# Kernel optimization log

Hardware: AMD Instinct MI355X
Metric: run time of the kernel (lower is better)

## Reference

```python
import jax, jax.numpy as jnp
import numpy as np
import math

HID = 512
HEADS = 8
DK = HID // HEADS
B, S, T = 8, 4096, 512


def setup_inputs() -> dict:
    key = jax.random.key(0)
    ks = jax.random.split(key, 12)
    scale = 0.02
    inp = {
        "inputs": jax.random.normal(ks[0], (B, S, HID), dtype=jnp.float32),
        "targets": jax.random.normal(ks[1], (B, T, HID), dtype=jnp.float32),
        "mask": jnp.ones((B, S), dtype=bool),
        "Wq": jax.random.normal(ks[2], (HID, HID), dtype=jnp.float32) * scale,
        "bq": jnp.zeros((HID,), dtype=jnp.float32),
        "Wk": jax.random.normal(ks[3], (HID, HID), dtype=jnp.float32) * scale,
        "bk": jnp.zeros((HID,), dtype=jnp.float32),
        "Wv": jax.random.normal(ks[4], (HID, HID), dtype=jnp.float32) * scale,
        "bv": jnp.zeros((HID,), dtype=jnp.float32),
        "Wo": jax.random.normal(ks[5], (HID, HID), dtype=jnp.float32) * scale,
        "bo": jnp.zeros((HID,), dtype=jnp.float32),
    }
    return inp


def reference(inputs, targets, mask, Wq, bq, Wk, bk, Wv, bv, Wo, bo):
    # PoolingFunction(method='multihead-attention'), dropout=0 (identity),
    # hidden_size == output_size so mapping_function is identity.
    b, t, h = targets.shape
    s = inputs.shape[1]
    Q = (targets @ Wq.T + bq).reshape(b, t, HEADS, DK)
    K = (inputs @ Wk.T + bk).reshape(b, s, HEADS, DK)
    V = (inputs @ Wv.T + bv).reshape(b, s, HEADS, DK)
    # scores: b x heads x tgt x seq (same math as (Q*K).sum(-1)/sqrt(d_k))
    e = jnp.einsum('bthd,bshd->bhts', Q, K) / math.sqrt(DK)
    neg = (1.0 - mask.astype(jnp.float32)) * -1e20  # b x s
    e = e + neg[:, None, None, :]
    a = jax.nn.softmax(e, axis=-1)  # softmax over seq dim
    ctx = jnp.einsum('bhts,bshd->bthd', a, V).reshape(b, t, h)
    return ctx @ Wo.T + bo
```

## Files before the change

### kernel.cpp

```cpp
#include <hip/hip_runtime.h>
#include <hip/hip_bf16.h>
#include <cstdint>
#include <cstddef>

#define HIDN   512
#define NHEADS 8
#define BATCH  8
#define SLEN   4096
#define TLEN   512
#define SSPLIT 4
#define SCHUNK (SLEN / SSPLIT)
#define SCL2   0.18033688f

typedef __attribute__((ext_vector_type(8))) short   bf16x8;
typedef __attribute__((ext_vector_type(4))) float   f32x4;
typedef unsigned short u16;
typedef unsigned int   u32;

__device__ __forceinline__ u32 pkbf(float a, float b) {
    __hip_bfloat162 h = __float22bfloat162_rn(float2{a, b});
    union { __hip_bfloat162 h; u32 u; } un; un.h = h; return un.u;
}
__device__ __forceinline__ u32 cvtpk(float a, float b) {
    u32 r;
    asm("v_cvt_pk_bf16_f32 %0, %1, %2" : "=v"(r) : "v"(a), "v"(b));
    return r;
}
__device__ __forceinline__ float fexp2(float x) {
    return __builtin_amdgcn_exp2f(x);
}
__device__ __forceinline__ void gload_lds16(const u16* g, u16* l) {
    __builtin_amdgcn_global_load_lds(
        (const __attribute__((address_space(1))) u32*)g,
        (__attribute__((address_space(3))) u32*)l, 16, 0, 0);
}

__global__ __launch_bounds__(256) void cvt_all(
    const float* __restrict__ X, const float* __restrict__ Tg,
    const float* __restrict__ Wq, const float* __restrict__ Wk,
    const float* __restrict__ Wv, const float* __restrict__ Wo,
    const int* __restrict__ mask,
    u16* __restrict__ Xc, u16* __restrict__ Tc, u16* __restrict__ Wc,
    float* __restrict__ negf)
{
    int i4 = blockIdx.x * 256 + threadIdx.x;
    if (i4 >= 4980736) {
        int off = i4 - 4980736;
        int4 mv = ((const int4*)mask)[off];
        float4 nv;
        nv.x = mv.x ? 0.f : -1e30f; nv.y = mv.y ? 0.f : -1e30f;
        nv.z = mv.z ? 0.f : -1e30f; nv.w = mv.w ? 0.f : -1e30f;
        ((float4*)negf)[off] = nv;
        return;
    }
    const float* s; u16* d; long off;
    if (i4 < 4194304)      { s = X;  d = Xc; off = i4; }
    else if (i4 < 4718592) { s = Tg; d = Tc; off = i4 - 4194304; }
    else {
        int wi = i4 - 4718592; int widx = wi >> 16;
        s = (widx == 0) ? Wq : (widx == 1) ? Wk : (widx == 2) ? Wv : Wo;
        d = Wc + widx * 262144; off = wi & 65535;
    }
    float4 v = *(const float4*)(s + off * 4);
    uint2 o; o.x = pkbf(v.x, v.y); o.y = pkbf(v.z, v.w);
    *(uint2*)(d + off * 4) = o;
}


template<int MODE, int SEQ>
__device__ __forceinline__ void gemmA_body(
    const u16* __restrict__ A, const u16* __restrict__ Bw,
    const float* __restrict__ bias, void* __restrict__ Yv,
    int m0, int n0, u16* As, u16* Bs)
{
    const int tid = threadIdx.x;
    const int lane = tid & 63;
    const int w = tid >> 6;
    const int m = lane & 15, qd = lane >> 4;
    const int wm = w >> 1, wn = w & 1;

    f32x4 acc[4][4];
#pragma unroll
    for (int i = 0; i < 4; ++i)
#pragma unroll
        for (int j = 0; j < 4; ++j) acc[i][j] = (f32x4){0.f, 0.f, 0.f, 0.f};

    for (int k0 = 0; k0 < HIDN; k0 += 32) {
#pragma unroll
        for (int r = 0; r < 2; ++r) {
            const int f = tid + r * 256;
            const int row = f >> 2, c8 = (f & 3) * 8;
            const int fb = f & ~63;
            gload_lds16(A  + (size_t)(m0 + row) * HIDN + k0 + c8, As + fb * 8);
            gload_lds16(Bw + (size_t)(n0 + row) * HIDN + k0 + c8, Bs + fb * 8);
        }
        __syncthreads();
        bf16x8 af[4], bf[4];
#pragma unroll
        for (int t = 0; t < 4; ++t) {
            af[t] = *(bf16x8*)&As[(64 * wm + 16 * t + m) * 32 + 8 * qd];
            bf[t] = *(bf16x8*)&Bs[(64 * wn + 16 * t + m) * 32 + 8 * qd];
        }
#pragma unroll
        for (int ti = 0; ti < 4; ++ti)
#pragma unroll
            for (int tj = 0; tj < 4; ++tj)
                acc[ti][tj] = __builtin_amdgcn_mfma_f32_16x16x32_bf16(
                    af[ti], bf[tj], acc[ti][tj], 0, 0, 0);
        __syncthreads();
    }

#pragma unroll
    for (int ti = 0; ti < 4; ++ti) {
        const int gr0 = m0 + 64 * wm + 16 * ti + 4 * qd;
#pragma unroll
        for (int tj = 0; tj < 4; ++tj) {
            const int gcol = n0 + 64 * wn + 16 * tj + m;
            const float bv = bias[gcol];
            if (MODE == 0) {
                float* Y = (float*)Yv;
#pragma unroll
                for (int i = 0; i < 4; ++i)
                    Y[(size_t)(gr0 + i) * HIDN + gcol] = acc[ti][tj][i] + bv;
            } else {
                u16* Y = (u16*)Yv;
                const int b = gr0 / SEQ, h = gcol >> 6, d = gcol & 63;
                const int r = gr0 & (SEQ - 1);
                uint2 o;
                o.x = pkbf(acc[ti][tj][0] + bv, acc[ti][tj][1] + bv);
                o.y = pkbf(acc[ti][tj][2] + bv, acc[ti][tj][3] + bv);
                *(uint2*)&Y[(((size_t)(b * 8 + h)) * 64 + d) * SEQ + r] = o;
            }
        }
    }
}

template<int SEQ>
__device__ __forceinline__ void wxT_body(
    const u16* __restrict__ Wm, const u16* __restrict__ X,
    const float* __restrict__ bias, u16* __restrict__ Y,
    int m0, int n0, u16* As, u16* Bs)
{
    const int tid = threadIdx.x;
    const int lane = tid & 63;
    const int w = tid >> 6;
    const int m = lane & 15, qd = lane >> 4;
    const int wm = w >> 1, wn = w & 1;

    f32x4 acc[4][4];
#pragma unroll
    for (int i = 0; i < 4; ++i)
#pragma unroll
        for (int j = 0; j < 4; ++j) acc[i][j] = (f32x4){0.f, 0.f, 0.f, 0.f};

    for (int k0 = 0; k0 < HIDN; k0 += 32) {
#pragma unroll
        for (int r = 0; r < 2; ++r) {
            const int f = tid + r * 256;
            const int row = f >> 2, c8 = (f & 3) * 8;
            const int fb = f & ~63;
            gload_lds16(Wm + (size_t)(m0 + row) * HIDN + k0 + c8, As + fb * 8);
            gload_lds16(X  + (size_t)(n0 + row) * HIDN + k0 + c8, Bs + fb * 8);
        }
        __syncthreads();
        bf16x8 af[4], bf[4];
#pragma unroll
        for (int t = 0; t < 4; ++t) {
            af[t] = *(bf16x8*)&As[(64 * wm + 16 * t + m) * 32 + 8 * qd];
            bf[t] = *(bf16x8*)&Bs[(64 * wn + 16 * t + m) * 32 + 8 * qd];
        }
#pragma unroll
        for (int ti = 0; ti < 4; ++ti)
#pragma unroll
            for (int tj = 0; tj < 4; ++tj)
                acc[ti][tj] = __builtin_amdgcn_mfma_f32_16x16x32_bf16(
                    af[ti], bf[tj], acc[ti][tj], 0, 0, 0);
        __syncthreads();
    }

#pragma unroll
    for (int ti = 0; ti < 4; ++ti) {
        const int o = m0 + 64 * wm + 16 * ti + 4 * qd;
        const float4 bv = *(const float4*)&bias[o];
        const int h = o >> 6, d0 = o & 63;
#pragma unroll
        for (int tj = 0; tj < 4; ++tj) {
            const int n = n0 + 64 * wn + 16 * tj + m;
            const int b = n / SEQ, r = n & (SEQ - 1);
            uint2 pk;
            pk.x = pkbf(acc[ti][tj][0] + bv.x, acc[ti][tj][1] + bv.y);
            pk.y = pkbf(acc[ti][tj][2] + bv.z, acc[ti][tj][3] + bv.w);
            *(uint2*)&Y[(((size_t)(b * 8 + h)) * SEQ + r) * 64 + d0] = pk;
        }
    }
}

__global__ __launch_bounds__(256)
void proj_all(const u16* __restrict__ Wc, const u16* __restrict__ Tc,
              const u16* __restrict__ Xc,
              const float* __restrict__ bq, const float* __restrict__ bk,
              const float* __restrict__ bv,
              u16* __restrict__ Qws, u16* __restrict__ Kws,
              u16* __restrict__ Vtws)
{
    __shared__ u16 As[128 * 32];
    __shared__ u16 Bs[128 * 32];
    const int bid = blockIdx.x;
    if (bid < 1024) {
        wxT_body<SLEN>(Wc + 262144, Xc, bk, Kws,
                       (bid >> 8) * 128, (bid & 255) * 128, As, Bs);
    } else if (bid < 2048) {
        const int b2 = bid - 1024;
        gemmA_body<2, SLEN>(Xc, Wc + 524288, bv, Vtws,
                            (b2 >> 2) * 128, (b2 & 3) * 128, As, Bs);
    } else {
        const int b2 = bid - 2048;
        wxT_body<TLEN>(Wc, Tc, bq, Qws,
                       (b2 >> 5) * 128, (b2 & 31) * 128, As, Bs);
    }
}

__global__ __launch_bounds__(256)
void gemm_out(const u16* __restrict__ A, const u16* __restrict__ Bw,
              const float* __restrict__ bias, float* __restrict__ Y)
{
    __shared__ u16 As[128 * 32];
    __shared__ u16 Bs[128 * 32];
    gemmA_body<0, TLEN>(A, Bw, bias, Y,
                        blockIdx.y * 128, blockIdx.x * 128, As, Bs);
}

__global__ __launch_bounds__(256, 2)
void attn_part(const u16* __restrict__ Q, const u16* __restrict__ K,
               const u16* __restrict__ Vt, const float* __restrict__ negf,
               float* __restrict__ Opart, float* __restrict__ lpart)
{
    __shared__ char Psh[32768];
    __shared__ u16  KVl[2][8192];
    __shared__ float Ngl[1024];
    const int tid = threadIdx.x;
    const int lane = tid & 63, w = tid >> 6;
    const int m = lane & 15, qd = lane >> 4;
    const int ti = blockIdx.x, si = blockIdx.y, bh = blockIdx.z;
    const int b = bh >> 3;

    const u16* Qp = Q + ((size_t)bh * TLEN + ti * 256) * 64;
    const u16* Kp = K + (size_t)bh * SLEN * 64;
    const u16* Vp = Vt + (size_t)bh * 64 * SLEN;
    const float* np = negf + (size_t)b * SLEN;
    const int s_beg = si * SCHUNK;

    const int sr = tid >> 3;
    const int sg = ((tid & 7) ^ (sr & 7)) * 8;
    const u16* kgb = Kp + (size_t)s_beg * 64 + sr * 64 + sg;
    const u16* vgb = Vp + s_beg + (size_t)sr * SLEN + sg;
    u16* kd = &KVl[0][0]    + tid * 8;
    u16* vd = &KVl[0][4096] + tid * 8;

#define STAGE(cc, bb) do {                                                   \
        const u16* kg_ = kgb + (size_t)(cc) * 4096;                          \
        const u16* vg_ = vgb + (cc) * 64;                                    \
        u16* kd_ = kd + (bb) * 8192;                                         \
        u16* vd_ = vd + (bb) * 8192;                                         \
        gload_lds16(kg_,                     kd_);                           \
        gload_lds16(kg_ + 32 * 64,           kd_ + 2048);                    \
        gload_lds16(vg_,                     vd_);                           \
        gload_lds16(vg_ + (size_t)32 * SLEN, vd_ + 2048);                    \
    } while (0)

    const int wb = w * 8192 + m * 128;
    int waddr[4], ra0[2], ra1[2];
#pragma unroll
    for (int st = 0; st < 4; ++st) waddr[st] = wb + (((4 * st + qd) ^ m) << 3);
#pragma unroll
    for (int ks = 0; ks < 2; ++ks) {
        const int u0 = 8 * ks + 2 * qd;
        ra0[ks] = wb + (((u0) ^ m) << 3);
        ra1[ks] = wb + (((u0 + 1) ^ m) << 3);
    }
    const int x0 = ((qd    ) ^ (m & 7)) * 8;
    const int x1 = ((4 + qd) ^ (m & 7)) * 8;

    bf16x8 qf[4][2];
#pragma unroll
    for (int ts = 0; ts < 4; ++ts)
#pragma unroll
        for (int kh = 0; kh < 2; ++kh)
            qf[ts][kh] = *(const bf16x8*)(Qp + (64 * w + 16 * ts + m) * 64 +
                                          32 * kh + 8 * qd);

    f32x4 O[4][4];
#pragma unroll
    for (int ts = 0; ts < 4; ++ts)
#pragma unroll
        for (int dt = 0; dt < 4; ++dt) O[ts][dt] = (f32x4){0.f, 0.f, 0.f, 0.f};
    float lr[4] = {0.f, 0.f, 0.f, 0.f};

#define CHUNK(cc) do {                                                       \
        const u16* Kl = &KVl[(cc) & 1][0];                                   \
        const u16* Vl = &KVl[(cc) & 1][4096];                                \
        bf16x8 kf[4][2];                                                     \
        _Pragma("unroll")                                                    \
        for (int st = 0; st < 4; ++st) {                                     \
            kf[st][0] = *(const bf16x8*)&Kl[st * 1024 + m * 64 + x0];        \
            kf[st][1] = *(const bf16x8*)&Kl[st * 1024 + m * 64 + x1];        \
        }                                                                    \
        float4 ng[4];                                                        \
        _Pragma("unroll")                                                    \
        for (int st = 0; st < 4; ++st)                                       \
            ng[st] = *(const float4*)&Ngl[((cc) << 6) + (st << 4) + (qd << 2)]; \
        _Pragma("unroll")                                                    \
        for (int ts = 0; ts < 4; ++ts) {                                     \
            f32x4 S[4];                                                      \
            _Pragma("unroll")                                                \
            for (int st = 0; st < 4; ++st) {                                 \
                f32x4 cc2 = (f32x4){0.f, 0.f, 0.f, 0.f};                     \
                cc2 = __builtin_amdgcn_mfma_f32_16x16x32_bf16(               \
                          kf[st][0], qf[ts][0], cc2, 0, 0, 0);               \
                cc2 = __builtin_amdgcn_mfma_f32_16x16x32_bf16(               \
                          kf[st][1], qf[ts][1], cc2, 0, 0, 0);               \
                S[st] = cc2;                                                 \
            }                                                                \
            float ls = 0.f;                                                  \
            _Pragma("unroll")                                                \
            for (int st = 0; st < 4; ++st) {                                 \
                const float p0 = fexp2(fmaf(S[st][0], SCL2, ng[st].x));      \
                const float p1 = fexp2(fmaf(S[st][1], SCL2, ng[st].y));      \
                const float p2 = fexp2(fmaf(S[st][2], SCL2, ng[st].z));      \
                const float p3 = fexp2(fmaf(S[st][3], SCL2, ng[st].w));      \
                ls += (p0 + p1) + (p2 + p3);                                 \
                *(uint2*)&Psh[waddr[st] + ts * 2048] =                       \
                    make_uint2(cvtpk(p0, p1), cvtpk(p2, p3));                \
            }                                                                \
            lr[ts] += ls;                                                    \
        }                                                                    \
        bf16x8 vf[4][2];                                                     \
        _Pragma("unroll")                                                    \
        for (int dt = 0; dt < 4; ++dt) {                                     \
            vf[dt][0] = *(const bf16x8*)&Vl[dt * 1024 + m * 64 + x0];        \
            vf[dt][1] = *(const bf16x8*)&Vl[dt * 1024 + m * 64 + x1];        \
        }                                                                    \
        __builtin_amdgcn_s_setprio(1);                                       \
        _Pragma("unroll")                                                    \
        for (int ts = 0; ts < 4; ++ts) {                                     \
            _Pragma("unroll")                                                \
            for (int ks = 0; ks < 2; ++ks) {                                 \
                const uint2 r0 = *(uint2*)&Psh[ra0[ks] + ts * 2048];         \
                const uint2 r1 = *(uint2*)&Psh[ra1[ks] + ts * 2048];         \
                union { uint4 u; bf16x8 v; } bu;                             \
                bu.u = make_uint4(r0.x, r0.y, r1.x, r1.y);                   \
                O[ts][0] = __builtin_amdgcn_mfma_f32_16x16x32_bf16(          \
                               vf[0][ks], bu.v, O[ts][0], 0, 0, 0);          \
                O[ts][1] = __builtin_amdgcn_mfma_f32_16x16x32_bf16(          \
                               vf[1][ks], bu.v, O[ts][1], 0, 0, 0);          \
                O[ts][2] = __builtin_amdgcn_mfma_f32_16x16x32_bf16(          \
                               vf[2][ks], bu.v, O[ts][2], 0, 0, 0);          \
                O[ts][3] = __builtin_amdgcn_mfma_f32_16x16x32_bf16(          \
                               vf[3][ks], bu.v, O[ts][3], 0, 0, 0);          \
            }                                                                \
        }                                                                    \
        __builtin_amdgcn_s_setprio(0);                                       \
    } while (0)

    STAGE(0, 0);
    gload_lds16((const u16*)(np + s_beg) + (size_t)tid * 8,
                ((u16*)Ngl) + tid * 8);
#pragma unroll 1
    for (int c = 0; c < (SCHUNK / 64) - 1; ++c) {
        STAGE(c + 1, (c + 1) & 1);
        asm volatile("s_waitcnt vmcnt(4)" ::: "memory");
        __builtin_amdgcn_s_barrier();
        __builtin_amdgcn_sched_barrier(0);
        CHUNK(c);
        __builtin_amdgcn_s_barrier();
        __builtin_amdgcn_sched_barrier(0);
    }
    asm volatile("s_waitcnt vmcnt(0)" ::: "memory");
    __builtin_amdgcn_s_barrier();
    __builtin_amdgcn_sched_barrier(0);
    CHUNK((SCHUNK / 64) - 1);

#undef STAGE
#undef CHUNK

#pragma unroll
    for (int ts = 0; ts < 4; ++ts) {
        float l = lr[ts];
        l += __shfl_xor(l, 16, 64);
        l += __shfl_xor(l, 32, 64);
        const int t = ti * 256 + 64 * w + 16 * ts + m;
        float* Ob = Opart + (((size_t)(si * 64 + bh)) * 512 + t) * 64;
#pragma unroll
        for (int dt = 0; dt < 4; ++dt)
            *(f32x4*)&Ob[16 * dt + 4 * qd] = O[ts][dt];
        if (qd == 0)
            lpart[((size_t)(si * 64 + bh)) * 512 + t] = l;
    }
}

__global__ __launch_bounds__(256)
void attn_combine(const float* __restrict__ Opart, const float* __restrict__ lpart,
                  u16* __restrict__ ctx)
{
    const int gid = blockIdx.x * 256 + threadIdx.x;
    const int d4 = gid & 15, t = (gid >> 4) & 511, bh = gid >> 13;
    const int b = bh >> 3, h = bh & 7;
    float4 o = {0.f, 0.f, 0.f, 0.f}; float l = 0.f;
#pragma unroll
    for (int si = 0; si < SSPLIT; ++si) {
        const size_t base = ((size_t)(si * 64 + bh)) * 512 + t;
        l += lpart[base];
        const float4 v = *(const float4*)(Opart + base * 64 + d4 * 4);
        o.x += v.x; o.y += v.y; o.z += v.z; o.w += v.w;
    }
    const float r = 1.f / l;
    uint2 pk; pk.x = pkbf(o.x * r, o.y * r); pk.y = pkbf(o.z * r, o.w * r);
    *(uint2*)&ctx[((size_t)(b * 512 + t)) * 512 + h * 64 + d4 * 4] = pk;
}

extern "C" void kernel_launch(void* const* d_in, const int* in_sizes, int n_in,
                              void* d_out, int out_size, void* d_ws, size_t ws_size,
                              hipStream_t stream)
{
    const float* inputs  = (const float*)d_in[0];
    const float* targets = (const float*)d_in[1];
    const int*   mask    = (const int*)d_in[2];
    const float* Wq = (const float*)d_in[3];
    const float* bq = (const float*)d_in[4];
    const float* Wk = (const float*)d_in[5];
    const float* bk = (const float*)d_in[6];
    const float* Wv = (const float*)d_in[7];
    const float* bv = (const float*)d_in[8];
    const float* Wo = (const float*)d_in[9];
    const float* bo = (const float*)d_in[10];

    char* ws = (char*)d_ws;
    u16*   Xc    = (u16*)(ws);
    u16*   Tc    = (u16*)(ws + 33554432);
    u16*   Wc    = (u16*)(ws + 37748736);
    float* negf  = (float*)(ws + 39845888);
    u16*   Qws   = (u16*)(ws + 39976960);
    u16*   Kws   = (u16*)(ws + 44171264);
    u16*   Vtws  = (u16*)(ws + 77725696);
    u16*   Cws   = (u16*)(ws + 111280128);
    float* Opart = (float*)(ws + 115474432);
    float* lpart = (float*)(ws + 149028864);

    cvt_all<<<19488, 256, 0, stream>>>(inputs, targets, Wq, Wk, Wv, Wo, mask,
                                       Xc, Tc, Wc, negf);

    proj_all<<<2176, 256, 0, stream>>>(Wc, Tc, Xc, bq, bk, bv,
                                       Qws, Kws, Vtws);

    attn_part<<<dim3(2, SSPLIT, 64), 256, 0, stream>>>(Qws, Kws, Vtws, negf,
                                                       Opart, lpart);
    attn_combine<<<2048, 256, 0, stream>>>(Opart, lpart, Cws);

    gemm_out<<<dim3(4, 32), 256, 0, stream>>>(Cws, Wc + 786432, bo,
                                              (float*)d_out);
}
```

Before: 258.9 us.

## Fuse fp32-to-bf16 activation conversion into projection GEMMs with double-buffered loads

Instead of first converting inputs and targets to bf16 in a separate pass, the projection GEMMs now read fp32 activations directly, convert them in registers and write them into LDS. The main loop is also rewritten with two LDS buffers and register prefetch of the next K-slice, plus explicit waitcnt and barrier scheduling. The goal is to drop the large conversion kernel's extra write and reread of the activations and to overlap loads with MFMA work. In exchange, each K and V tile block rereads fp32 activations, which is twice the bytes of bf16, across the weight-tile blocks, and uses more LDS and registers.

```diff
diff --git a/kernel.cpp b/kernel.cpp
--- a/kernel.cpp
+++ b/kernel.cpp
@@ -36,16 +36,15 @@
 }
 
 __global__ __launch_bounds__(256) void cvt_all(
-    const float* __restrict__ X, const float* __restrict__ Tg,
     const float* __restrict__ Wq, const float* __restrict__ Wk,
     const float* __restrict__ Wv, const float* __restrict__ Wo,
     const int* __restrict__ mask,
-    u16* __restrict__ Xc, u16* __restrict__ Tc, u16* __restrict__ Wc,
-    float* __restrict__ negf)
+    u16* __restrict__ Wc, float* __restrict__ negf)
 {
     int i4 = blockIdx.x * 256 + threadIdx.x;
-    if (i4 >= 4980736) {
-        int off = i4 - 4980736;
+    if (i4 >= 262144) {
+        int off = i4 - 262144;
+        if (off >= 8192) return;
         int4 mv = ((const int4*)mask)[off];
         float4 nv;
         nv.x = mv.x ? 0.f : -1e30f; nv.y = mv.y ? 0.f : -1e30f;
@@ -53,31 +52,201 @@
         ((float4*)negf)[off] = nv;
         return;
     }
-    const float* s; u16* d; long off;
-    if (i4 < 4194304)      { s = X;  d = Xc; off = i4; }
-    else if (i4 < 4718592) { s = Tg; d = Tc; off = i4 - 4194304; }
-    else {
-        int wi = i4 - 4718592; int widx = wi >> 16;
-        s = (widx == 0) ? Wq : (widx == 1) ? Wk : (widx == 2) ? Wv : Wo;
-        d = Wc + widx * 262144; off = wi & 65535;
-    }
+    int widx = i4 >> 16;
+    const float* s = (widx == 0) ? Wq : (widx == 1) ? Wk : (widx == 2) ? Wv : Wo;
+    u16* d = Wc + widx * 262144;
+    long off = i4 & 65535;
     float4 v = *(const float4*)(s + off * 4);
     uint2 o; o.x = pkbf(v.x, v.y); o.y = pkbf(v.z, v.w);
     *(uint2*)(d + off * 4) = o;
 }
 
-
-template<int MODE, int SEQ>
-__device__ __forceinline__ void gemmA_body(
-    const u16* __restrict__ A, const u16* __restrict__ Bw,
-    const float* __restrict__ bias, void* __restrict__ Yv,
-    int m0, int n0, u16* As, u16* Bs)
+template<bool F32_IS_A>
+__device__ __forceinline__ void mix_gemm(
+    const u16* __restrict__ bp, const float* __restrict__ fp,
+    int brow0, int frow0, u16 (*As)[4096], u16 (*Bs)[4096],
+    f32x4 (&acc)[4][4])
 {
     const int tid = threadIdx.x;
-    const int lane = tid & 63;
-    const int w = tid >> 6;
+    const int lane = tid & 63, w = tid >> 6;
     const int m = lane & 15, qd = lane >> 4;
     const int wm = w >> 1, wn = w & 1;
+    const int b0r = tid >> 2,         b0c = (tid & 3) * 8,  b0d = (tid & ~63) * 8;
+    const int b1r = (tid + 256) >> 2, b1d = ((tid + 256) & ~63) * 8;
+    const int fr = tid >> 3, fq = tid & 7;
+    u16 (*BD)[4096] = F32_IS_A ? Bs : As;
+    u16 (*FD)[4096] = F32_IS_A ? As : Bs;
+    float4 RA[4], RB[4];
+
+#define MISSUE(k0, bb, R) do {                                               \
+        gload_lds16(bp + (size_t)(brow0 + b0r) * HIDN + (k0) + b0c,          \
+                    &BD[bb][0] + b0d);                                       \
+        gload_lds16(bp + (size_t)(brow0 + b1r) * HIDN + (k0) + b0c,          \
+                    &BD[bb][0] + b1d);                                       \
+        _Pragma("unroll")                                                    \
+        for (int j = 0; j < 4; ++j)                                          \
+            R[j] = *(const float4*)(fp +                                     \
+                    (size_t)(frow0 + fr + 32 * j) * HIDN + (k0) + 4 * fq);   \
+    } while (0)
+
+#define MWRITE(bb, R) do {                                                   \
+        _Pragma("unroll")                                                    \
+        for (int j = 0; j < 4; ++j) {                                        \
+            uint2 o; o.x = pkbf(R[j].x, R[j].y); o.y = pkbf(R[j].z, R[j].w); \
+            *(uint2*)&FD[bb][(fr + 32 * j) * 32 + fq * 4] = o;               \
+        }                                                                    \
+    } while (0)
+
+#define MCOMP(bb) do {                                                       \
+        bf16x8 af[4], bf[4];                                                 \
+        _Pragma("unroll")                                                    \
+        for (int t = 0; t < 4; ++t) {                                        \
+            af[t] = *(bf16x8*)&As[bb][(64 * wm + 16 * t + m) * 32 + 8 * qd]; \
+            bf[t] = *(bf16x8*)&Bs[bb][(64 * wn + 16 * t + m) * 32 + 8 * qd]; \
+        }                                                                    \
+        _Pragma("unroll")                                                    \
+        for (int ti2 = 0; ti2 < 4; ++ti2)                                    \
+            _Pragma("unroll")                                                \
+            for (int tj = 0; tj < 4; ++tj)                                   \
+                acc[ti2][tj] = __builtin_amdgcn_mfma_f32_16x16x32_bf16(      \
+                    af[ti2], bf[tj], acc[ti2][tj], 0, 0, 0);                 \
+    } while (0)
+
+#define MSTEP(c, bb, RCUR, RNXT, LAST) do {                                  \
+        if (!(LAST)) MISSUE(((c) + 1) * 32, (bb) ^ 1, RNXT);                 \
+        if (LAST) asm volatile("s_waitcnt vmcnt(0)" ::: "memory");           \
+        else      asm volatile("s_waitcnt vmcnt(6)" ::: "memory");           \
+        MWRITE(bb, RCUR);                                                    \
+        asm volatile("s_waitcnt lgkmcnt(0)" ::: "memory");                   \
+        __builtin_amdgcn_s_barrier();                                        \
+        __builtin_amdgcn_sched_barrier(0);                                   \
+        MCOMP(bb);                                                           \
+        __builtin_amdgcn_s_barrier();                                        \
+        __builtin_amdgcn_sched_barrier(0);                                   \
+    } while (0)
+
+    MISSUE(0, 0, RA);
+#pragma unroll 1
+    for (int cc = 0; cc < 7; ++cc) {
+        MSTEP(2 * cc,     0, RA, RB, 0);
+        MSTEP(2 * cc + 1, 1, RB, RA, 0);
+    }
+    MSTEP(14, 0, RA, RB, 0);
+    MSTEP(15, 1, RB, RA, 1);
+
+#undef MISSUE
+#undef MWRITE
+#undef MCOMP
+#undef MSTEP
+}
+
+template<int SEQ>
+__device__ __forceinline__ void mixK_body(
+    const u16* __restrict__ Wm, const float* __restrict__ Xf,
+    const float* __restrict__ bias, u16* __restrict__ Y,
+    int m0, int n0, u16 (*As)[4096], u16 (*Bs)[4096])
+{
+    const int tid = threadIdx.x;
+    const int lane = tid & 63, w = tid >> 6;
+    const int m = lane & 15, qd = lane >> 4;
+    const int wm = w >> 1, wn = w & 1;
+
+    f32x4 acc[4][4];
+#pragma unroll
+    for (int i = 0; i < 4; ++i)
+#pragma unroll
+        for (int j = 0; j < 4; ++j) acc[i][j] = (f32x4){0.f, 0.f, 0.f, 0.f};
+
+    mix_gemm<false>(Wm, Xf, m0, n0, As, Bs, acc);
+
+#pragma unroll
+    for (int ti = 0; ti < 4; ++ti) {
+        const int o = m0 + 64 * wm + 16 * ti + 4 * qd;
+        const float4 bv = *(const float4*)&bias[o];
+        const int h = o >> 6, d0 = o & 63;
+#pragma unroll
+        for (int tj = 0; tj < 4; ++tj) {
+            const int n = n0 + 64 * wn + 16 * tj + m;
+            const int b = n / SEQ, r = n & (SEQ - 1);
+            uint2 pk;
+            pk.x = pkbf(acc[ti][tj][0] + bv.x, acc[ti][tj][1] + bv.y);
+            pk.y = pkbf(acc[ti][tj][2] + bv.z, acc[ti][tj][3] + bv.w);
+            *(uint2*)&Y[(((size_t)(b * 8 + h)) * SEQ + r) * 64 + d0] = pk;
+        }
+    }
+}
+
+__device__ __forceinline__ void mixV_body(
+    const float* __restrict__ Xf, const u16* __restrict__ Bw,
+    const float* __restrict__ bias, u16* __restrict__ Y,
+    int m0, int n0, u16 (*As)[4096], u16 (*Bs)[4096])
+{
+    const int tid = threadIdx.x;
+    const int lane = tid & 63, w = tid >> 6;
+    const int m = lane & 15, qd = lane >> 4;
+    const int wm = w >> 1, wn = w & 1;
+
+    f32x4 acc[4][4];
+#pragma unroll
+    for (int i = 0; i < 4; ++i)
+#pragma unroll
+        for (int j = 0; j < 4; ++j) acc[i][j] = (f32x4){0.f, 0.f, 0.f, 0.f};
+
+    mix_gemm<true>(Bw, Xf, n0, m0, As, Bs, acc);
+
+#pragma unroll
+    for (int ti = 0; ti < 4; ++ti) {
+        const int gr0 = m0 + 64 * wm + 16 * ti + 4 * qd;
+#pragma unroll
+        for (int tj = 0; tj < 4; ++tj) {
+            const int gcol = n0 + 64 * wn + 16 * tj + m;
+            const float bv = bias[gcol];
+            const int b = gr0 / SLEN, h = gcol >> 6, d = gcol & 63;
+            const int r = gr0 & (SLEN - 1);
+            uint2 o;
+            o.x = pkbf(acc[ti][tj][0] + bv, acc[ti][tj][1] + bv);
+            o.y = pkbf(acc[ti][tj][2] + bv, acc[ti][tj][3] + bv);
+            *(uint2*)&Y[(((size_t)(b * 8 + h)) * 64 + d) * SLEN + r] = o;
+        }
+    }
+}
+
+__global__ __launch_bounds__(256)
+void proj_all(const u16* __restrict__ Wc,
+              const float* __restrict__ Xf, const float* __restrict__ Tf,
+              const float* __restrict__ bq, const float* __restrict__ bk,
+              const float* __restrict__ bv,
+              u16* __restrict__ Qws, u16* __restrict__ Kws,
+              u16* __restrict__ Vtws)
+{
+    __shared__ u16 As[2][4096];
+    __shared__ u16 Bs[2][4096];
+    const int bid = blockIdx.x;
+    if (bid < 1024) {
+        mixK_body<SLEN>(Wc + 262144, Xf, bk, Kws,
+                        (bid >> 8) * 128, (bid & 255) * 128, As, Bs);
+    } else if (bid < 2048) {
+        const int b2 = bid - 1024;
+        mixV_body(Xf, Wc + 524288, bv, Vtws,
+                  (b2 >> 2) * 128, (b2 & 3) * 128, As, Bs);
+    } else {
+        const int b2 = bid - 2048;
+        mixK_body<TLEN>(Wc, Tf, bq, Qws,
+                        (b2 >> 5) * 128, (b2 & 31) * 128, As, Bs);
+    }
+}
+
+__global__ __launch_bounds__(256)
+void gemm_out(const u16* __restrict__ A, const u16* __restrict__ Bw,
+              const float* __restrict__ bias, float* __restrict__ Y)
+{
+    __shared__ u16 As[128 * 32];
+    __shared__ u16 Bs[128 * 32];
+    const int tid = threadIdx.x;
+    const int lane = tid & 63, w = tid >> 6;
+    const int m = lane & 15, qd = lane >> 4;
+    const int wm = w >> 1, wn = w & 1;
+    const int m0 = blockIdx.y * 128, n0 = blockIdx.x * 128;
 
     f32x4 acc[4][4];
 #pragma unroll
@@ -117,117 +286,11 @@
         for (int tj = 0; tj < 4; ++tj) {
             const int gcol = n0 + 64 * wn + 16 * tj + m;
             const float bv = bias[gcol];
-            if (MODE == 0) {
-                float* Y = (float*)Yv;
-#pragma unroll
-                for (int i = 0; i < 4; ++i)
-                    Y[(size_t)(gr0 + i) * HIDN + gcol] = acc[ti][tj][i] + bv;
-            } else {
-                u16* Y = (u16*)Yv;
-                const int b = gr0 / SEQ, h = gcol >> 6, d = gcol & 63;
-                const int r = gr0 & (SEQ - 1);
-                uint2 o;
-                o.x = pkbf(acc[ti][tj][0] + bv, acc[ti][tj][1] + bv);
-                o.y = pkbf(acc[ti][tj][2] + bv, acc[ti][tj][3] + bv);
-                *(uint2*)&Y[(((size_t)(b * 8 + h)) * 64 + d) * SEQ + r] = o;
-            }
+#pragma unroll
+            for (int i = 0; i < 4; ++i)
+                Y[(size_t)(gr0 + i) * HIDN + gcol] = acc[ti][tj][i] + bv;
         }
     }
-}
-
-template<int SEQ>
-__device__ __forceinline__ void wxT_body(
-    const u16* __restrict__ Wm, const u16* __restrict__ X,
-    const float* __restrict__ bias, u16* __restrict__ Y,
-    int m0, int n0, u16* As, u16* Bs)
-{
-    const int tid = threadIdx.x;
-    const int lane = tid & 63;
-    const int w = tid >> 6;
-    const int m = lane & 15, qd = lane >> 4;
-    const int wm = w >> 1, wn = w & 1;
-
-    f32x4 acc[4][4];
-#pragma unroll
-    for (int i = 0; i < 4; ++i)
-#pragma unroll
-        for (int j = 0; j < 4; ++j) acc[i][j] = (f32x4){0.f, 0.f, 0.f, 0.f};
-
-    for (int k0 = 0; k0 < HIDN; k0 += 32) {
-#pragma unroll
-        for (int r = 0; r < 2; ++r) {
-            const int f = tid + r * 256;
-            const int row = f >> 2, c8 = (f & 3) * 8;
-            const int fb = f & ~63;
-            gload_lds16(Wm + (size_t)(m0 + row) * HIDN + k0 + c8, As + fb * 8);
-            gload_lds16(X  + (size_t)(n0 + row) * HIDN + k0 + c8, Bs + fb * 8);
-        }
-        __syncthreads();
-        bf16x8 af[4], bf[4];
-#pragma unroll
-        for (int t = 0; t < 4; ++t) {
-            af[t] = *(bf16x8*)&As[(64 * wm + 16 * t + m) * 32 + 8 * qd];
-            bf[t] = *(bf16x8*)&Bs[(64 * wn + 16 * t + m) * 32 + 8 * qd];
-        }
-#pragma unroll
-        for (int ti = 0; ti < 4; ++ti)
-#pragma unroll
-            for (int tj = 0; tj < 4; ++tj)
-                acc[ti][tj] = __builtin_amdgcn_mfma_f32_16x16x32_bf16(
-                    af[ti], bf[tj], acc[ti][tj], 0, 0, 0);
-        __syncthreads();
-    }
-
-#pragma unroll
-    for (int ti = 0; ti < 4; ++ti) {
-        const int o = m0 + 64 * wm + 16 * ti + 4 * qd;
-        const float4 bv = *(const float4*)&bias[o];
-        const int h = o >> 6, d0 = o & 63;
-#pragma unroll
-        for (int tj = 0; tj < 4; ++tj) {
-            const int n = n0 + 64 * wn + 16 * tj + m;
-            const int b = n / SEQ, r = n & (SEQ - 1);
-            uint2 pk;
-            pk.x = pkbf(acc[ti][tj][0] + bv.x, acc[ti][tj][1] + bv.y);
-            pk.y = pkbf(acc[ti][tj][2] + bv.z, acc[ti][tj][3] + bv.w);
-            *(uint2*)&Y[(((size_t)(b * 8 + h)) * SEQ + r) * 64 + d0] = pk;
-        }
-    }
-}
-
-__global__ __launch_bounds__(256)
-void proj_all(const u16* __restrict__ Wc, const u16* __restrict__ Tc,
-              const u16* __restrict__ Xc,
-              const float* __restrict__ bq, const float* __restrict__ bk,
-              const float* __restrict__ bv,
-              u16* __restrict__ Qws, u16* __restrict__ Kws,
-              u16* __restrict__ Vtws)
-{
-    __shared__ u16 As[128 * 32];
-    __shared__ u16 Bs[128 * 32];
-    const int bid = blockIdx.x;
-    if (bid < 1024) {
-        wxT_body<SLEN>(Wc + 262144, Xc, bk, Kws,
-                       (bid >> 8) * 128, (bid & 255) * 128, As, Bs);
-    } else if (bid < 2048) {
-        const int b2 = bid - 1024;
-        gemmA_body<2, SLEN>(Xc, Wc + 524288, bv, Vtws,
-                            (b2 >> 2) * 128, (b2 & 3) * 128, As, Bs);
-    } else {
-        const int b2 = bid - 2048;
-        wxT_body<TLEN>(Wc, Tc, bq, Qws,
-                       (b2 >> 5) * 128, (b2 & 31) * 128, As, Bs);
-    }
-}
-
-__global__ __launch_bounds__(256)
-void gemm_out(const u16* __restrict__ A, const u16* __restrict__ Bw,
-              const float* __restrict__ bias, float* __restrict__ Y)
-{
-    __shared__ u16 As[128 * 32];
-    __shared__ u16 Bs[128 * 32];
-    gemmA_body<0, TLEN>(A, Bw, bias, Y,
-                        blockIdx.y * 128, blockIdx.x * 128, As, Bs);
 }
 
 __global__ __launch_bounds__(256, 2)
@@ -435,8 +498,6 @@
     const float* bo = (const float*)d_in[10];
 
     char* ws = (char*)d_ws;
-    u16*   Xc    = (u16*)(ws);
-    u16*   Tc    = (u16*)(ws + 33554432);
     u16*   Wc    = (u16*)(ws + 37748736);
     float* negf  = (float*)(ws + 39845888);
     u16*   Qws   = (u16*)(ws + 39976960);
@@ -446,10 +507,9 @@
     float* Opart = (float*)(ws + 115474432);
     float* lpart = (float*)(ws + 149028864);
 
-    cvt_all<<<19488, 256, 0, stream>>>(inputs, targets, Wq, Wk, Wv, Wo, mask,
-                                       Xc, Tc, Wc, negf);
-
-    proj_all<<<2176, 256, 0, stream>>>(Wc, Tc, Xc, bq, bk, bv,
+    cvt_all<<<1056, 256, 0, stream>>>(Wq, Wk, Wv, Wo, mask, Wc, negf);
+
+    proj_all<<<2176, 256, 0, stream>>>(Wc, inputs, targets, bq, bk, bv,
                                        Qws, Kws, Vtws);
 
     attn_part<<<dim3(2, SSPLIT, 64), 256, 0, stream>>>(Qws, Kws, Vtws, negf,
```

Measured after the change: 290.0 us. +12.0%, slower.

## Fuse split-softmax combine into output GEMM and widen projection K-tiles with swizzle

Applied to the files above, without the earlier changes.

Removes the attn_combine kernel. The output projection GEMM now reads the four partial O/l buffers, reduces and normalizes them, converts to bf16 and writes the A tile into LDS itself, so the ctx round trip through global memory is gone. The projection GEMMs also move to 64-wide K tiles with an XOR-swizzled LDS layout, which halves the number of barrier iterations and is meant to cut bank conflicts. The cost is that each of the 128 output blocks redundantly re-reads Opart across the four column blocks, and the fused A-load is not overlapped with compute.

```diff
diff --git a/kernel.cpp b/kernel.cpp
--- a/kernel.cpp
+++ b/kernel.cpp
@@ -66,86 +66,59 @@
     *(uint2*)(d + off * 4) = o;
 }
 
-
-template<int MODE, int SEQ>
-__device__ __forceinline__ void gemmA_body(
-    const u16* __restrict__ A, const u16* __restrict__ Bw,
-    const float* __restrict__ bias, void* __restrict__ Yv,
-    int m0, int n0, u16* As, u16* Bs)
-{
-    const int tid = threadIdx.x;
-    const int lane = tid & 63;
-    const int w = tid >> 6;
-    const int m = lane & 15, qd = lane >> 4;
-    const int wm = w >> 1, wn = w & 1;
-
-    f32x4 acc[4][4];
-#pragma unroll
-    for (int i = 0; i < 4; ++i)
-#pragma unroll
-        for (int j = 0; j < 4; ++j) acc[i][j] = (f32x4){0.f, 0.f, 0.f, 0.f};
-
-    for (int k0 = 0; k0 < HIDN; k0 += 32) {
-#pragma unroll
-        for (int r = 0; r < 2; ++r) {
-            const int f = tid + r * 256;
-            const int row = f >> 2, c8 = (f & 3) * 8;
-            const int fb = f & ~63;
-            gload_lds16(A  + (size_t)(m0 + row) * HIDN + k0 + c8, As + fb * 8);
-            gload_lds16(Bw + (size_t)(n0 + row) * HIDN + k0 + c8, Bs + fb * 8);
-        }
-        __syncthreads();
-        bf16x8 af[4], bf[4];
-#pragma unroll
-        for (int t = 0; t < 4; ++t) {
-            af[t] = *(bf16x8*)&As[(64 * wm + 16 * t + m) * 32 + 8 * qd];
-            bf[t] = *(bf16x8*)&Bs[(64 * wn + 16 * t + m) * 32 + 8 * qd];
-        }
-#pragma unroll
-        for (int ti = 0; ti < 4; ++ti)
-#pragma unroll
-            for (int tj = 0; tj < 4; ++tj)
-                acc[ti][tj] = __builtin_amdgcn_mfma_f32_16x16x32_bf16(
-                    af[ti], bf[tj], acc[ti][tj], 0, 0, 0);
-        __syncthreads();
-    }
-
-#pragma unroll
-    for (int ti = 0; ti < 4; ++ti) {
-        const int gr0 = m0 + 64 * wm + 16 * ti + 4 * qd;
-#pragma unroll
-        for (int tj = 0; tj < 4; ++tj) {
-            const int gcol = n0 + 64 * wn + 16 * tj + m;
-            const float bv = bias[gcol];
-            if (MODE == 0) {
-                float* Y = (float*)Yv;
-#pragma unroll
-                for (int i = 0; i < 4; ++i)
-                    Y[(size_t)(gr0 + i) * HIDN + gcol] = acc[ti][tj][i] + bv;
-            } else {
-                u16* Y = (u16*)Yv;
-                const int b = gr0 / SEQ, h = gcol >> 6, d = gcol & 63;
-                const int r = gr0 & (SEQ - 1);
-                uint2 o;
-                o.x = pkbf(acc[ti][tj][0] + bv, acc[ti][tj][1] + bv);
-                o.y = pkbf(acc[ti][tj][2] + bv, acc[ti][tj][3] + bv);
-                *(uint2*)&Y[(((size_t)(b * 8 + h)) * 64 + d) * SEQ + r] = o;
-            }
-        }
-    }
-}
+#define G64_DECLS                                                            \
+    const int sR = tid >> 3;                                                 \
+    const int sG = ((tid & 7) ^ (sR & 7)) * 8;                               \
+    const int sB = (tid & ~63) * 8
+
+#define G64_STAGE(P, row0, k0, D) do {                                       \
+        _Pragma("unroll")                                                    \
+        for (int r = 0; r < 4; ++r)                                          \
+            gload_lds16(P + (size_t)((row0) + sR + 32 * r) * HIDN            \
+                          + (k0) + sG,                                       \
+                        D + sB + r * 2048);                                  \
+    } while (0)
+
+#define G64_READ(SRC, wq, t_, kh)                                            \
+    (*(bf16x8*)&SRC[(64 * (wq) + 16 * (t_) + m) * 64 +                       \
+                    ((4 * (kh) + qd) ^ (m & 7)) * 8])
+
+#define G64_LOOP(Aptr, Bptr) do {                                            \
+        _Pragma("unroll 1")                                                  \
+        for (int c = 0; c < 8; ++c) {                                        \
+            G64_STAGE(Aptr, m0, 64 * c, As);                                 \
+            G64_STAGE(Bptr, n0, 64 * c, Bs);                                 \
+            __syncthreads();                                                 \
+            _Pragma("unroll")                                                \
+            for (int kh = 0; kh < 2; ++kh) {                                 \
+                bf16x8 af[4], bf[4];                                         \
+                _Pragma("unroll")                                            \
+                for (int t = 0; t < 4; ++t) {                                \
+                    af[t] = G64_READ(As, wm, t, kh);                         \
+                    bf[t] = G64_READ(Bs, wn, t, kh);                         \
+                }                                                            \
+                _Pragma("unroll")                                            \
+                for (int ti = 0; ti < 4; ++ti)                               \
+                    _Pragma("unroll")                                        \
+                    for (int tj = 0; tj < 4; ++tj)                           \
+                        acc[ti][tj] = __builtin_amdgcn_mfma_f32_16x16x32_bf16(\
+                            af[ti], bf[tj], acc[ti][tj], 0, 0, 0);           \
+            }                                                                \
+            __syncthreads();                                                 \
+        }                                                                    \
+    } while (0)
 
 template<int SEQ>
-__device__ __forceinline__ void wxT_body(
+__device__ __forceinline__ void wxT64_body(
     const u16* __restrict__ Wm, const u16* __restrict__ X,
     const float* __restrict__ bias, u16* __restrict__ Y,
     int m0, int n0, u16* As, u16* Bs)
 {
     const int tid = threadIdx.x;
-    const int lane = tid & 63;
-    const int w = tid >> 6;
+    const int lane = tid & 63, w = tid >> 6;
     const int m = lane & 15, qd = lane >> 4;
     const int wm = w >> 1, wn = w & 1;
+    G64_DECLS;
 
     f32x4 acc[4][4];
 #pragma unroll
@@ -153,30 +126,7 @@
 #pragma unroll
         for (int j = 0; j < 4; ++j) acc[i][j] = (f32x4){0.f, 0.f, 0.f, 0.f};
 
-    for (int k0 = 0; k0 < HIDN; k0 += 32) {
-#pragma unroll
-        for (int r = 0; r < 2; ++r) {
-            const int f = tid + r * 256;
-            const int row = f >> 2, c8 = (f & 3) * 8;
-            const int fb = f & ~63;
-            gload_lds16(Wm + (size_t)(m0 + row) * HIDN + k0 + c8, As + fb * 8);
-            gload_lds16(X  + (size_t)(n0 + row) * HIDN + k0 + c8, Bs + fb * 8);
-        }
-        __syncthreads();
-        bf16x8 af[4], bf[4];
-#pragma unroll
-        for (int t = 0; t < 4; ++t) {
-            af[t] = *(bf16x8*)&As[(64 * wm + 16 * t + m) * 32 + 8 * qd];
-            bf[t] = *(bf16x8*)&Bs[(64 * wn + 16 * t + m) * 32 + 8 * qd];
-        }
-#pragma unroll
-        for (int ti = 0; ti < 4; ++ti)
-#pragma unroll
-            for (int tj = 0; tj < 4; ++tj)
-                acc[ti][tj] = __builtin_amdgcn_mfma_f32_16x16x32_bf16(
-                    af[ti], bf[tj], acc[ti][tj], 0, 0, 0);
-        __syncthreads();
-    }
+    G64_LOOP(Wm, X);
 
 #pragma unroll
     for (int ti = 0; ti < 4; ++ti) {
@@ -195,6 +145,42 @@
     }
 }
 
+__device__ __forceinline__ void vproj64_body(
+    const u16* __restrict__ A, const u16* __restrict__ Bw,
+    const float* __restrict__ bias, u16* __restrict__ Y,
+    int m0, int n0, u16* As, u16* Bs)
+{
+    const int tid = threadIdx.x;
+    const int lane = tid & 63, w = tid >> 6;
+    const int m = lane & 15, qd = lane >> 4;
+    const int wm = w >> 1, wn = w & 1;
+    G64_DECLS;
+
+    f32x4 acc[4][4];
+#pragma unroll
+    for (int i = 0; i < 4; ++i)
+#pragma unroll
+        for (int j = 0; j < 4; ++j) acc[i][j] = (f32x4){0.f, 0.f, 0.f, 0.f};
+
+    G64_LOOP(A, Bw);
+
+#pragma unroll
+    for (int ti = 0; ti < 4; ++ti) {
+        const int gr0 = m0 + 64 * wm + 16 * ti + 4 * qd;
+#pragma unroll
+        for (int tj = 0; tj < 4; ++tj) {
+            const int gcol = n0 + 64 * wn + 16 * tj + m;
+            const float bv = bias[gcol];
+            const int b = gr0 / SLEN, h = gcol >> 6, d = gcol & 63;
+            const int r = gr0 & (SLEN - 1);
+            uint2 o;
+            o.x = pkbf(acc[ti][tj][0] + bv, acc[ti][tj][1] + bv);
+            o.y = pkbf(acc[ti][tj][2] + bv, acc[ti][tj][3] + bv);
+            *(uint2*)&Y[(((size_t)(b * 8 + h)) * 64 + d) * SLEN + r] = o;
+        }
+    }
+}
+
 __global__ __launch_bounds__(256)
 void proj_all(const u16* __restrict__ Wc, const u16* __restrict__ Tc,
               const u16* __restrict__ Xc,
@@ -203,31 +189,118 @@
               u16* __restrict__ Qws, u16* __restrict__ Kws,
               u16* __restrict__ Vtws)
 {
+    __shared__ u16 As[128 * 64];
+    __shared__ u16 Bs[128 * 64];
+    const int bid = blockIdx.x;
+    if (bid < 1024) {
+        wxT64_body<SLEN>(Wc + 262144, Xc, bk, Kws,
+                         (bid >> 8) * 128, (bid & 255) * 128, As, Bs);
+    } else if (bid < 2048) {
+        const int b2 = bid - 1024;
+        vproj64_body(Xc, Wc + 524288, bv, Vtws,
+                     (b2 >> 2) * 128, (b2 & 3) * 128, As, Bs);
+    } else {
+        const int b2 = bid - 2048;
+        wxT64_body<TLEN>(Wc, Tc, bq, Qws,
+                         (b2 >> 5) * 128, (b2 & 31) * 128, As, Bs);
+    }
+}
+
+__global__ __launch_bounds__(256)
+void gemm_out_fused(const float* __restrict__ Opart,
+                    const float* __restrict__ lpart,
+                    const u16* __restrict__ Bw, const float* __restrict__ bias,
+                    float* __restrict__ Y)
+{
     __shared__ u16 As[128 * 32];
     __shared__ u16 Bs[128 * 32];
-    const int bid = blockIdx.x;
-    if (bid < 1024) {
-        wxT_body<SLEN>(Wc + 262144, Xc, bk, Kws,
-                       (bid >> 8) * 128, (bid & 255) * 128, As, Bs);
-    } else if (bid < 2048) {
-        const int b2 = bid - 1024;
-        gemmA_body<2, SLEN>(Xc, Wc + 524288, bv, Vtws,
-                            (b2 >> 2) * 128, (b2 & 3) * 128, As, Bs);
-    } else {
-        const int b2 = bid - 2048;
-        wxT_body<TLEN>(Wc, Tc, bq, Qws,
-                       (b2 >> 5) * 128, (b2 & 31) * 128, As, Bs);
-    }
-}
-
-__global__ __launch_bounds__(256)
-void gemm_out(const u16* __restrict__ A, const u16* __restrict__ Bw,
-              const float* __restrict__ bias, float* __restrict__ Y)
-{
-    __shared__ u16 As[128 * 32];
-    __shared__ u16 Bs[128 * 32];
-    gemmA_body<0, TLEN>(A, Bw, bias, Y,
-                        blockIdx.y * 128, blockIdx.x * 128, As, Bs);
+    const int tid = threadIdx.x;
+    const int lane = tid & 63, w = tid >> 6;
+    const int m = lane & 15, qd = lane >> 4;
+    const int wm = w >> 1, wn = w & 1;
+    const int m0 = blockIdx.y * 128, n0 = blockIdx.x * 128;
+    const int fr = tid >> 3, fq = tid & 7;
+
+    f32x4 acc[4][4];
+#pragma unroll
+    for (int i = 0; i < 4; ++i)
+#pragma unroll
+        for (int j = 0; j < 4; ++j) acc[i][j] = (f32x4){0.f, 0.f, 0.f, 0.f};
+
+#pragma unroll 1
+    for (int h = 0; h < 8; ++h) {
+        float invl[4];
+#pragma unroll
+        for (int j = 0; j < 4; ++j) {
+            const int gr = m0 + fr + 32 * j;
+            const int b = gr >> 9, t = gr & 511;
+            const size_t lb = ((size_t)(b * 8 + h)) * 512 + t;
+            float l = lpart[lb];
+            l += lpart[lb + 1 * 64 * 512];
+            l += lpart[lb + 2 * 64 * 512];
+            l += lpart[lb + 3 * 64 * 512];
+            invl[j] = 1.f / l;
+        }
+#pragma unroll
+        for (int kk = 0; kk < 2; ++kk) {
+            const int k0 = h * 64 + kk * 32;
+            {
+                const int f0 = tid, r0 = f0 >> 2, c8 = (f0 & 3) * 8;
+                gload_lds16(Bw + (size_t)(n0 + r0) * HIDN + k0 + c8,
+                            Bs + (f0 & ~63) * 8);
+                const int f1 = tid + 256, r1 = f1 >> 2;
+                gload_lds16(Bw + (size_t)(n0 + r1) * HIDN + k0 + c8,
+                            Bs + (f1 & ~63) * 8);
+            }
+#pragma unroll
+            for (int j = 0; j < 4; ++j) {
+                const int gr = m0 + fr + 32 * j;
+                const int b = gr >> 9, t = gr & 511;
+                const size_t ob = (((size_t)(b * 8 + h)) * 512 + t) * 64
+                                  + kk * 32 + fq * 4;
+                const float4 v0 = *(const float4*)(Opart + ob);
+                const float4 v1 = *(const float4*)(Opart + ob + (size_t)1 * 2097152);
+                const float4 v2 = *(const float4*)(Opart + ob + (size_t)2 * 2097152);
+                const float4 v3 = *(const float4*)(Opart + ob + (size_t)3 * 2097152);
+                float sx = v0.x; sx += v1.x; sx += v2.x; sx += v3.x;
+                float sy = v0.y; sy += v1.y; sy += v2.y; sy += v3.y;
+                float sz = v0.z; sz += v1.z; sz += v2.z; sz += v3.z;
+                float sw = v0.w; sw += v1.w; sw += v2.w; sw += v3.w;
+                const float r = invl[j];
+                uint2 pk;
+                pk.x = pkbf(sx * r, sy * r);
+                pk.y = pkbf(sz * r, sw * r);
+                *(uint2*)&As[(fr + 32 * j) * 32 + fq * 4] = pk;
+            }
+            __syncthreads();
+            bf16x8 af[4], bf[4];
+#pragma unroll
+            for (int t = 0; t < 4; ++t) {
+                af[t] = *(bf16x8*)&As[(64 * wm + 16 * t + m) * 32 + 8 * qd];
+                bf[t] = *(bf16x8*)&Bs[(64 * wn + 16 * t + m) * 32 + 8 * qd];
+            }
+#pragma unroll
+            for (int ti = 0; ti < 4; ++ti)
+#pragma unroll
+                for (int tj = 0; tj < 4; ++tj)
+                    acc[ti][tj] = __builtin_amdgcn_mfma_f32_16x16x32_bf16(
+                        af[ti], bf[tj], acc[ti][tj], 0, 0, 0);
+            __syncthreads();
+        }
+    }
+
+#pragma unroll
+    for (int ti = 0; ti < 4; ++ti) {
+        const int gr0 = m0 + 64 * wm + 16 * ti + 4 * qd;
+#pragma unroll
+        for (int tj = 0; tj < 4; ++tj) {
+            const int gcol = n0 + 64 * wn + 16 * tj + m;
+            const float bv = bias[gcol];
+#pragma unroll
+            for (int i = 0; i < 4; ++i)
+                Y[(size_t)(gr0 + i) * HIDN + gcol] = acc[ti][tj][i] + bv;
+        }
+    }
 }
 
 __global__ __launch_bounds__(256, 2)
@@ -398,26 +471,6 @@
     }
 }
 
-__global__ __launch_bounds__(256)
-void attn_combine(const float* __restrict__ Opart, const float* __restrict__ lpart,
-                  u16* __restrict__ ctx)
-{
-    const int gid = blockIdx.x * 256 + threadIdx.x;
-    const int d4 = gid & 15, t = (gid >> 4) & 511, bh = gid >> 13;
-    const int b = bh >> 3, h = bh & 7;
-    float4 o = {0.f, 0.f, 0.f, 0.f}; float l = 0.f;
-#pragma unroll
-    for (int si = 0; si < SSPLIT; ++si) {
-        const size_t base = ((size_t)(si * 64 + bh)) * 512 + t;
-        l += lpart[base];
-        const float4 v = *(const float4*)(Opart + base * 64 + d4 * 4);
-        o.x += v.x; o.y += v.y; o.z += v.z; o.w += v.w;
-    }
-    const float r = 1.f / l;
-    uint2 pk; pk.x = pkbf(o.x * r, o.y * r); pk.y = pkbf(o.z * r, o.w * r);
-    *(uint2*)&ctx[((size_t)(b * 512 + t)) * 512 + h * 64 + d4 * 4] = pk;
-}
-
 extern "C" void kernel_launch(void* const* d_in, const int* in_sizes, int n_in,
                               void* d_out, int out_size, void* d_ws, size_t ws_size,
                               hipStream_t stream)
@@ -442,7 +495,6 @@
     u16*   Qws   = (u16*)(ws + 39976960);
     u16*   Kws   = (u16*)(ws + 44171264);
     u16*   Vtws  = (u16*)(ws + 77725696);
-    u16*   Cws   = (u16*)(ws + 111280128);
     float* Opart = (float*)(ws + 115474432);
     float* lpart = (float*)(ws + 149028864);
 
@@ -454,8 +506,8 @@
 
     attn_part<<<dim3(2, SSPLIT, 64), 256, 0, stream>>>(Qws, Kws, Vtws, negf,
                                                        Opart, lpart);
-    attn_combine<<<2048, 256, 0, stream>>>(Opart, lpart, Cws);
-
-    gemm_out<<<dim3(4, 32), 256, 0, stream>>>(Cws, Wc + 786432, bo,
-                                              (float*)d_out);
-}
+
+    gemm_out_fused<<<dim3(4, 32), 256, 0, stream>>>(Opart, lpart,
+                                                    Wc + 786432, bo,
+                                                    (float*)d_out);
+}
```

After: 299.9 us. 15.8% more time.
